# Performance work log

Hardware: AMD Instinct MI355X
Metric: run time of the kernel (lower is better)

The kernel has to match this reference:

```python
import jax, jax.numpy as jnp
import numpy as np

NB_HEAD = 8
SIZE_PER_HEAD = 64
MAX_LEN = 1024
D_IN = 512
BATCH = 8
NEG_BIG = 1e12  # matches the torch module's mask * 1000000000000.0


def setup_inputs() -> dict:
    key = jax.random.key(0)
    ks = jax.random.split(key, 6)
    return {
        "Q_seq": jax.random.normal(ks[0], (BATCH, MAX_LEN, D_IN), dtype=jnp.float32),
        "K_seq": jax.random.normal(ks[1], (BATCH, MAX_LEN, D_IN), dtype=jnp.float32),
        "V_seq": jax.random.normal(ks[2], (BATCH, MAX_LEN, D_IN), dtype=jnp.float32),
        "WQ": jax.random.normal(ks[3], (D_IN, NB_HEAD * SIZE_PER_HEAD), dtype=jnp.float32),
        "WK": jax.random.normal(ks[4], (D_IN, NB_HEAD * SIZE_PER_HEAD), dtype=jnp.float32),
        "WV": jax.random.normal(ks[5], (D_IN, NB_HEAD * SIZE_PER_HEAD), dtype=jnp.float32),
    }


def reference(Q_seq, K_seq, V_seq, WQ, WK, WV):
    B, L, _ = Q_seq.shape
    H, D = NB_HEAD, SIZE_PER_HEAD
    # QKV projections -> [B, H, L, D]
    q = (Q_seq @ WQ).reshape(B, L, H, D).transpose(0, 2, 1, 3)
    k = (K_seq @ WK).reshape(B, L, H, D).transpose(0, 2, 1, 3)
    v = (V_seq @ WV).reshape(B, L, H, D).transpose(0, 2, 1, 3)
    # scaled dot-product scores [B, H, Lq, Lk]
    scores = jnp.einsum("bhqd,bhkd->bhqk", q, k) / jnp.sqrt(jnp.float32(D))
    # causal mask: the torch Mask() subtracts 1e12 where key_idx > query_idx
    causal = jnp.triu(jnp.ones((L, L), dtype=scores.dtype), k=1)  # 1 where k > q
    scores = scores - causal[None, None, :, :] * NEG_BIG
    attn = jax.nn.softmax(scores, axis=-1)
    out = jnp.einsum("bhqk,bhkd->bhqd", attn, v)  # [B, H, L, D]
    return out.transpose(0, 2, 1, 3).reshape(B, L, H * D)
```

## Files before the change

kernel.cpp:

```cpp
#include <hip/hip_runtime.h>
#include <cstddef>

#define LEN    1024
#define DIN    512
#define NHEAD  8
#define HDIM   64
#define BATCH  8

typedef __attribute__((ext_vector_type(8))) short  short8;
typedef __attribute__((ext_vector_type(4))) float  f32x4;

#define MFMA16(a, b, c) __builtin_amdgcn_mfma_f32_16x16x32_bf16((a), (b), (c), 0, 0, 0)
#define PERM_HI 0x07060302u
#define PERM_LO 0x05040100u

__device__ __forceinline__ unsigned short bf_hi(float x) {
    unsigned u = __float_as_uint(x);
    return (unsigned short)((u + 0x7fffu + ((u >> 16) & 1u)) >> 16);
}
__device__ __forceinline__ void bf_split(float x, unsigned short& h, unsigned short& l) {
    unsigned u  = __float_as_uint(x);
    unsigned hu = (u + 0x7fffu + ((u >> 16) & 1u)) >> 16;
    h = (unsigned short)hu;
    l = bf_hi(x - __uint_as_float(hu << 16));
}
__device__ __forceinline__ void unpack4(uint4 u, ushort4& h, ushort4& l) {
    h = make_ushort4((unsigned short)(u.x >> 16), (unsigned short)(u.y >> 16),
                     (unsigned short)(u.z >> 16), (unsigned short)(u.w >> 16));
    l = make_ushort4((unsigned short)(u.x & 0xffff), (unsigned short)(u.y & 0xffff),
                     (unsigned short)(u.z & 0xffff), (unsigned short)(u.w & 0xffff));
}
__device__ __forceinline__ void unpack8(uint4 a, uint4 b, uint4& h, uint4& l) {
    h = make_uint4(__builtin_amdgcn_perm(a.y, a.x, PERM_HI),
                   __builtin_amdgcn_perm(a.w, a.z, PERM_HI),
                   __builtin_amdgcn_perm(b.y, b.x, PERM_HI),
                   __builtin_amdgcn_perm(b.w, b.z, PERM_HI));
    l = make_uint4(__builtin_amdgcn_perm(a.y, a.x, PERM_LO),
                   __builtin_amdgcn_perm(a.w, a.z, PERM_LO),
                   __builtin_amdgcn_perm(b.y, b.x, PERM_LO),
                   __builtin_amdgcn_perm(b.w, b.z, PERM_LO));
}

template<int CTRL>
__device__ __forceinline__ float dpp_mov(float x) {
    return __int_as_float(__builtin_amdgcn_update_dpp(
        0, __float_as_int(x), CTRL, 0xF, 0xF, true));
}
__device__ __forceinline__ float red16_max(float x) {
    x = fmaxf(x, dpp_mov<0xB1>(x));
    x = fmaxf(x, dpp_mov<0x4E>(x));
    x = fmaxf(x, dpp_mov<0x141>(x));
    x = fmaxf(x, dpp_mov<0x140>(x));
    return x;
}
__device__ __forceinline__ float red16_sum(float x) {
    x += dpp_mov<0xB1>(x);
    x += dpp_mov<0x4E>(x);
    x += dpp_mov<0x141>(x);
    x += dpp_mov<0x140>(x);
    return x;
}

__global__ __launch_bounds__(256)
void wprep(const float* __restrict__ WQ, const float* __restrict__ WK,
           const float* __restrict__ WV, unsigned short* __restrict__ wt)
{
    __shared__ float T[64][68];
    const int z = blockIdx.z;
    const float* W = (z == 0) ? WQ : (z == 1) ? WK : WV;
    unsigned short* Wth = wt + (size_t)z * 524288;
    unsigned short* Wtl = Wth + 262144;
    const int k0 = blockIdx.x * 64, n0 = blockIdx.y * 64;
    const int t = threadIdx.x;
    #pragma unroll
    for (int e = 0; e < 4; ++e) {
        int f = e * 256 + t, r = f >> 4, c4 = (f & 15) << 2;
        *(float4*)&T[r][c4] = *(const float4*)&W[(size_t)(k0 + r) * 512 + n0 + c4];
    }
    __syncthreads();
    #pragma unroll
    for (int e = 0; e < 4; ++e) {
        int f = e * 256 + t, nr = f >> 4, kc4 = (f & 15) << 2;
        ushort4 h, l;
        bf_split(T[kc4 + 0][nr], h.x, l.x);
        bf_split(T[kc4 + 1][nr], h.y, l.y);
        bf_split(T[kc4 + 2][nr], h.z, l.z);
        bf_split(T[kc4 + 3][nr], h.w, l.w);
        *(ushort4*)&Wth[(size_t)(n0 + nr) * 512 + k0 + kc4] = h;
        *(ushort4*)&Wtl[(size_t)(n0 + nr) * 512 + k0 + kc4] = l;
    }
}

#define PSTR 40

__global__ __launch_bounds__(256, 3)
void proj_mfma(const float* __restrict__ Qin, const float* __restrict__ Kin,
               const float* __restrict__ Vin, const unsigned short* __restrict__ wt,
               unsigned int* __restrict__ qhl, unsigned int* __restrict__ khl,
               unsigned short* __restrict__ vh)
{
    __shared__ unsigned short Ah[128 * PSTR], Al[128 * PSTR],
                              Bh[128 * PSTR], Bl[128 * PSTR];
    const int z = blockIdx.z;
    const bool full = (z < 2);
    const float* X = (z == 0) ? Qin : (z == 1) ? Kin : Vin;
    const unsigned short* Wth = wt + (size_t)z * 524288;
    const unsigned short* Wtl = Wth + 262144;

    const int t = threadIdx.x, lane = t & 63, w = t >> 6;
    const int wm = w & 1, wn = w >> 1;
    const int m0 = blockIdx.x * 128, n0 = blockIdx.y * 128;
    const int lm = lane & 15, lq = lane >> 4;
    const int ar = t >> 1, ak = (t & 1) * 16;

    const float* Xp = X + (size_t)(m0 + ar) * 512 + ak;
    const unsigned short* Bph = Wth + (size_t)(n0 + ar) * 512 + ak;
    const unsigned short* Bpl = Wtl + (size_t)(n0 + ar) * 512 + ak;

    f32x4 acc[4][4];
    #pragma unroll
    for (int i = 0; i < 4; ++i)
        #pragma unroll
        for (int j = 0; j < 4; ++j) acc[i][j] = 0.f;

    float4 av[4];
    uint4 bh0, bh1, bl0, bl1;
    #pragma unroll
    for (int e = 0; e < 4; ++e) av[e] = *(const float4*)(Xp + e * 4);
    bh0 = *(const uint4*)(Bph);
    bh1 = *(const uint4*)(Bph + 8);
    if (full) { bl0 = *(const uint4*)(Bpl); bl1 = *(const uint4*)(Bpl + 8); }

    for (int k0 = 0; k0 < 512; k0 += 32) {
        __syncthreads();
        {
            const float* ff = (const float*)&av[0];
            uint hw[16];
            #pragma unroll
            for (int i = 0; i < 16; ++i) hw[i] = __float_as_uint(ff[i]) & 0xffff0000u;
            uint4 ahv  = make_uint4(__builtin_amdgcn_perm(hw[1],  hw[0],  PERM_HI),
                                    __builtin_amdgcn_perm(hw[3],  hw[2],  PERM_HI),
                                    __builtin_amdgcn_perm(hw[5],  hw[4],  PERM_HI),
                                    __builtin_amdgcn_perm(hw[7],  hw[6],  PERM_HI));
            uint4 ahv2 = make_uint4(__builtin_amdgcn_perm(hw[9],  hw[8],  PERM_HI),
                                    __builtin_amdgcn_perm(hw[11], hw[10], PERM_HI),
                                    __builtin_amdgcn_perm(hw[13], hw[12], PERM_HI),
                                    __builtin_amdgcn_perm(hw[15], hw[14], PERM_HI));
            *(uint4*)&Ah[ar * PSTR + ak]     = ahv;
            *(uint4*)&Ah[ar * PSTR + ak + 8] = ahv2;
            if (full) {
                uint lo[8];
                #pragma unroll
                for (int i = 0; i < 8; ++i) {
                    float r0 = ff[2*i]   - __uint_as_float(hw[2*i]);
                    float r1 = ff[2*i+1] - __uint_as_float(hw[2*i+1]);
                    lo[i] = ((uint)bf_hi(r1) << 16) | bf_hi(r0);
                }
                *(uint4*)&Al[ar * PSTR + ak]     = make_uint4(lo[0], lo[1], lo[2], lo[3]);
                *(uint4*)&Al[ar * PSTR + ak + 8] = make_uint4(lo[4], lo[5], lo[6], lo[7]);
            }
        }
        *(uint4*)&Bh[ar * PSTR + ak]     = bh0;
        *(uint4*)&Bh[ar * PSTR + ak + 8] = bh1;
        if (full) {
            *(uint4*)&Bl[ar * PSTR + ak]     = bl0;
            *(uint4*)&Bl[ar * PSTR + ak + 8] = bl1;
        }
        __syncthreads();

        if (k0 + 32 < 512) {
            #pragma unroll
            for (int e = 0; e < 4; ++e) av[e] = *(const float4*)(Xp + k0 + 32 + e * 4);
            bh0 = *(const uint4*)(Bph + k0 + 32);
            bh1 = *(const uint4*)(Bph + k0 + 40);
            if (full) {
                bl0 = *(const uint4*)(Bpl + k0 + 32);
                bl1 = *(const uint4*)(Bpl + k0 + 40);
            }
        }

        short8 a_h[4], a_l[4];
        #pragma unroll
        for (int mi = 0; mi < 4; ++mi) {
            int off = (wm * 64 + mi * 16 + lm) * PSTR + lq * 8;
            a_h[mi] = *(const short8*)&Ah[off];
            if (full) a_l[mi] = *(const short8*)&Al[off];
        }
        #pragma unroll
        for (int ni = 0; ni < 4; ++ni) {
            int off = (wn * 64 + ni * 16 + lm) * PSTR + lq * 8;
            short8 b_h = *(const short8*)&Bh[off];
            if (full) {
                short8 b_l = *(const short8*)&Bl[off];
                #pragma unroll
                for (int mi = 0; mi < 4; ++mi) {
                    acc[mi][ni] = MFMA16(a_l[mi], b_h, acc[mi][ni]);
                    acc[mi][ni] = MFMA16(a_h[mi], b_l, acc[mi][ni]);
                    acc[mi][ni] = MFMA16(a_h[mi], b_h, acc[mi][ni]);
                }
            } else {
                #pragma unroll
                for (int mi = 0; mi < 4; ++mi)
                    acc[mi][ni] = MFMA16(a_h[mi], b_h, acc[mi][ni]);
            }
        }
    }

    if (z < 2) {
        unsigned int* o = (z == 0) ? qhl : khl;
        const float sc = (z == 0) ? 0.18033688011112042f : 1.0f;
        #pragma unroll
        for (int mi = 0; mi < 4; ++mi)
            #pragma unroll
            for (int ni = 0; ni < 4; ++ni) {
                int n_abs = n0 + wn * 64 + ni * 16 + lm;
                int hd = n_abs >> 6, d = n_abs & 63;
                #pragma unroll
                for (int r = 0; r < 4; ++r) {
                    int m_abs = m0 + wm * 64 + mi * 16 + lq * 4 + r;
                    int b = m_abs >> 10, li = m_abs & 1023;
                    unsigned short hv, lv;
                    bf_split(acc[mi][ni][r] * sc, hv, lv);
                    o[(((size_t)b * NHEAD + hd) * LEN + li) * HDIM + d] =
                        ((unsigned)hv << 16) | lv;
                }
            }
    } else {
        #pragma unroll
        for (int mi = 0; mi < 4; ++mi) {
            int m_base = m0 + wm * 64 + mi * 16 + lq * 4;
            int b = m_base >> 10, l0 = m_base & 1023;
            #pragma unroll
            for (int ni = 0; ni < 4; ++ni) {
                int n_abs = n0 + wn * 64 + ni * 16 + lm;
                int hd = n_abs >> 6, d = n_abs & 63;
                ushort4 hv = make_ushort4(bf_hi(acc[mi][ni][0]), bf_hi(acc[mi][ni][1]),
                                          bf_hi(acc[mi][ni][2]), bf_hi(acc[mi][ni][3]));
                *(ushort4*)&vh[(((size_t)b * NHEAD + hd) * HDIM + d) * LEN + l0] = hv;
            }
        }
    }
}

__global__ __launch_bounds__(256)
void attn_mfma(const unsigned int* __restrict__ qhl, const unsigned int* __restrict__ khl,
               const unsigned short* __restrict__ vth, float* __restrict__ out)
{
    __shared__ unsigned short sm[18432];
    unsigned short* Kh  = sm;
    unsigned short* Kl  = sm + 4608;
    unsigned short* Pb  = sm;
    unsigned short* Vt  = sm + 9216;
    unsigned short* Qsh = sm;
    unsigned short* Qsl = sm + 9216;

    const int t = threadIdx.x, lane = t & 63, w = t >> 6;
    const int lm = lane & 15, lq = lane >> 4;
    const int bx = blockIdx.x;
    const int idx = bx >> 1, par = bx & 1;
    const int bh = idx & 63;
    const int a  = idx >> 6;
    const int qt = par ? (7 - a) : a;
    const size_t base = (size_t)bh * LEN * HDIM;
    const unsigned int*   qb = qhl + base;
    const unsigned int*   kb = khl + base;
    const unsigned short* vb = vth + base;
    const int Q0  = qt * 128;
    const int Q0w = Q0 + w * 32;

    #pragma unroll
    for (int e = 0; e < 8; ++e) {
        int f = e * 256 + t, r = f >> 4, c4 = (f & 15) << 2;
        uint4 u = *(const uint4*)&qb[(size_t)(Q0 + r) * 64 + c4];
        ushort4 h, l;
        unpack4(u, h, l);
        *(ushort4*)&Qsh[r * 72 + c4] = h;
        *(ushort4*)&Qsl[r * 72 + c4] = l;
    }
    __syncthreads();
    short8 qfh[2][2], qfl[2][2];
    #pragma unroll
    for (int mi = 0; mi < 2; ++mi)
        #pragma unroll
        for (int ks = 0; ks < 2; ++ks) {
            int off = (w * 32 + mi * 16 + lm) * 72 + ks * 32 + lq * 8;
            qfh[mi][ks] = *(const short8*)&Qsh[off];
            qfl[mi][ks] = *(const short8*)&Qsl[off];
        }

    float m_i[2][4], l_i[2][4];
    f32x4 oacc[2][4];
    #pragma unroll
    for (int mi = 0; mi < 2; ++mi)
        #pragma unroll
        for (int r = 0; r < 4; ++r) { m_i[mi][r] = -1e30f; l_i[mi][r] = 0.f; }
    #pragma unroll
    for (int mi = 0; mi < 2; ++mi)
        #pragma unroll
        for (int nd = 0; nd < 4; ++nd) oacc[mi][nd] = 0.f;

    const int kr = t >> 2, kq = t & 3;
    const int vd_ = t >> 3, vs8 = (t & 7) << 3;

    uint4 kreg[4], vreg[2];
    #pragma unroll
    for (int e = 0; e < 4; ++e)
        kreg[e] = *(const uint4*)&kb[(size_t)kr * 64 + kq * 16 + e * 4];
    #pragma unroll
    for (int e = 0; e < 2; ++e)
        vreg[e] = *(const uint4*)&vb[(size_t)(e * 32 + vd_) * LEN + vs8];

    const int jend = 2 * qt + 1;
    for (int jb = 0; jb <= jend; ++jb) {
        __syncthreads();
        {
            uint4 h0, l0, h1, l1;
            unpack8(kreg[0], kreg[1], h0, l0);
            unpack8(kreg[2], kreg[3], h1, l1);
            int ko = kr * 72 + kq * 16;
            *(uint4*)&Kh[ko]     = h0;
            *(uint4*)&Kh[ko + 8] = h1;
            *(uint4*)&Kl[ko]     = l0;
            *(uint4*)&Kl[ko + 8] = l1;
            *(uint4*)&Vt[(vd_)      * 72 + vs8] = vreg[0];
            *(uint4*)&Vt[(vd_ + 32) * 72 + vs8] = vreg[1];
        }
        __syncthreads();

        if (jb < jend) {
            #pragma unroll
            for (int e = 0; e < 4; ++e)
                kreg[e] = *(const uint4*)&kb[(size_t)((jb + 1) * 64 + kr) * 64 + kq * 16 + e * 4];
            #pragma unroll
            for (int e = 0; e < 2; ++e)
                vreg[e] = *(const uint4*)&vb[(size_t)(e * 32 + vd_) * LEN + (jb + 1) * 64 + vs8];
        }

        const bool active = (jb * 64 <= Q0w + 31);
        f32x4 sf[2][4];
        if (active) {
            #pragma unroll
            for (int mi = 0; mi < 2; ++mi)
                #pragma unroll
                for (int ni = 0; ni < 4; ++ni) sf[mi][ni] = 0.f;
            #pragma unroll
            for (int ks = 0; ks < 2; ++ks)
                #pragma unroll
                for (int ni = 0; ni < 4; ++ni) {
                    int off = (ni * 16 + lm) * 72 + ks * 32 + lq * 8;
                    short8 b_h = *(const short8*)&Kh[off];
                    short8 b_l = *(const short8*)&Kl[off];
                    #pragma unroll
                    for (int mi = 0; mi < 2; ++mi) {
                        sf[mi][ni] = MFMA16(qfl[mi][ks], b_h, sf[mi][ni]);
                        sf[mi][ni] = MFMA16(qfh[mi][ks], b_l, sf[mi][ni]);
                        sf[mi][ni] = MFMA16(qfh[mi][ks], b_h, sf[mi][ni]);
                    }
                }
            if (jb * 64 + 63 > Q0w) {
                #pragma unroll
                for (int mi = 0; mi < 2; ++mi)
                    #pragma unroll
                    for (int ni = 0; ni < 4; ++ni) {
                        int key = jb * 64 + ni * 16 + lm;
                        #pragma unroll
                        for (int r = 0; r < 4; ++r) {
                            int qi = Q0w + mi * 16 + lq * 4 + r;
                            if (key > qi) sf[mi][ni][r] = -1e30f;
                        }
                    }
            }
        }
        __syncthreads();

        if (active) {
            #pragma unroll
            for (int mi = 0; mi < 2; ++mi)
                #pragma unroll
                for (int r = 0; r < 4; ++r) {
                    float mv = fmaxf(fmaxf(sf[mi][0][r], sf[mi][1][r]),
                                     fmaxf(sf[mi][2][r], sf[mi][3][r]));
                    mv = red16_max(mv);
                    float mo = m_i[mi][r];
                    float mn = fmaxf(mo, mv);
                    float al = __builtin_amdgcn_exp2f(mo - mn);
                    m_i[mi][r] = mn;
                    float rs = 0.f;
                    int prow = (w * 32 + mi * 16 + lq * 4 + r) * 72 + lm;
                    #pragma unroll
                    for (int ni = 0; ni < 4; ++ni) {
                        float p = __builtin_amdgcn_exp2f(sf[mi][ni][r] - mn);
                        rs += p;
                        Pb[prow + ni * 16] = bf_hi(p);
                    }
                    rs = red16_sum(rs);
                    l_i[mi][r] = l_i[mi][r] * al + rs;
                    #pragma unroll
                    for (int nd = 0; nd < 4; ++nd) oacc[mi][nd][r] *= al;
                }
            short8 pf[2][2];
            #pragma unroll
            for (int mi = 0; mi < 2; ++mi)
                #pragma unroll
                for (int ks = 0; ks < 2; ++ks)
                    pf[mi][ks] = *(const short8*)&Pb[(w * 32 + mi * 16 + lm) * 72 + ks * 32 + lq * 8];
            #pragma unroll
            for (int ks = 0; ks < 2; ++ks)
                #pragma unroll
                for (int nd = 0; nd < 4; ++nd) {
                    short8 vf = *(const short8*)&Vt[(nd * 16 + lm) * 72 + ks * 32 + lq * 8];
                    #pragma unroll
                    for (int mi = 0; mi < 2; ++mi)
                        oacc[mi][nd] = MFMA16(pf[mi][ks], vf, oacc[mi][nd]);
                }
        }
    }

    const int b = bh >> 3, hd = bh & 7;
    #pragma unroll
    for (int mi = 0; mi < 2; ++mi)
        #pragma unroll
        for (int r = 0; r < 4; ++r) {
            int qrow = Q0w + mi * 16 + lq * 4 + r;
            float inv = 1.0f / l_i[mi][r];
            #pragma unroll
            for (int nd = 0; nd < 4; ++nd) {
                int d = nd * 16 + lm;
                out[((size_t)b * LEN + qrow) * (NHEAD * HDIM) + hd * 64 + d] =
                    oacc[mi][nd][r] * inv;
            }
        }
}

extern "C" void kernel_launch(void* const* d_in, const int* in_sizes, int n_in,
                              void* d_out, int out_size, void* d_ws, size_t ws_size,
                              hipStream_t stream)
{
    const float* Qin = (const float*)d_in[0];
    const float* Kin = (const float*)d_in[1];
    const float* Vin = (const float*)d_in[2];
    const float* WQ  = (const float*)d_in[3];
    const float* WK  = (const float*)d_in[4];
    const float* WV  = (const float*)d_in[5];

    const size_t per = (size_t)BATCH * NHEAD * LEN * HDIM;
    unsigned int*   qhl = (unsigned int*)d_ws;
    unsigned int*   khl = qhl + per;
    unsigned short* vh  = (unsigned short*)(khl + per);
    unsigned short* wt  = vh + per;

    wprep    <<<dim3(8, 8, 3),  256, 0, stream>>>(WQ, WK, WV, wt);
    proj_mfma<<<dim3(64, 4, 3), 256, 0, stream>>>(Qin, Kin, Vin, wt, qhl, khl, vh);
    attn_mfma<<<dim3(512),      256, 0, stream>>>(qhl, khl, vh, (float*)d_out);
}
```

Measured before the change: 188.0 us.

## Transpose attention MFMA operands so each lane owns a query row

Swaps the MFMA A/B operands for QK^T and PV so score and output accumulators are laid out with one query row per lane. The row max and sum then need only two cross-lane shuffles instead of a 16-lane DPP reduction per element, and the running m/l state shrinks to one value per row tile. P gets its own XOR-swizzled LDS region, written as packed bf16 pairs, so one __syncthreads per key block can be dropped. The output is stored as float4 vectors, and launch bounds now request 3 blocks per CU. The trade-off is a larger shared-memory footprint and possible register pressure from the occupancy hint.

```diff
diff --git a/kernel.cpp b/kernel.cpp
--- a/kernel.cpp
+++ b/kernel.cpp
@@ -40,25 +40,8 @@
                    __builtin_amdgcn_perm(b.y, b.x, PERM_LO),
                    __builtin_amdgcn_perm(b.w, b.z, PERM_LO));
 }
-
-template<int CTRL>
-__device__ __forceinline__ float dpp_mov(float x) {
-    return __int_as_float(__builtin_amdgcn_update_dpp(
-        0, __float_as_int(x), CTRL, 0xF, 0xF, true));
-}
-__device__ __forceinline__ float red16_max(float x) {
-    x = fmaxf(x, dpp_mov<0xB1>(x));
-    x = fmaxf(x, dpp_mov<0x4E>(x));
-    x = fmaxf(x, dpp_mov<0x141>(x));
-    x = fmaxf(x, dpp_mov<0x140>(x));
-    return x;
-}
-__device__ __forceinline__ float red16_sum(float x) {
-    x += dpp_mov<0xB1>(x);
-    x += dpp_mov<0x4E>(x);
-    x += dpp_mov<0x141>(x);
-    x += dpp_mov<0x140>(x);
-    return x;
+__device__ __forceinline__ short8 as_s8(uint4 u) {
+    union { uint4 u; short8 s; } x; x.u = u; return x.s;
 }
 
 __global__ __launch_bounds__(256)
@@ -242,15 +225,15 @@
     }
 }
 
-__global__ __launch_bounds__(256)
+__global__ __launch_bounds__(256, 3)
 void attn_mfma(const unsigned int* __restrict__ qhl, const unsigned int* __restrict__ khl,
                const unsigned short* __restrict__ vth, float* __restrict__ out)
 {
-    __shared__ unsigned short sm[18432];
-    unsigned short* Kh  = sm;
-    unsigned short* Kl  = sm + 4608;
-    unsigned short* Pb  = sm;
-    unsigned short* Vt  = sm + 9216;
+    __shared__ unsigned short sm[23040];
+    unsigned short* Kh = sm;
+    unsigned short* Kl = sm + 4608;
+    unsigned short* Vt = sm + 9216;
+    unsigned int*   Pb = (unsigned int*)(sm + 13824);
     unsigned short* Qsh = sm;
     unsigned short* Qsl = sm + 9216;
 
@@ -288,16 +271,15 @@
             qfl[mi][ks] = *(const short8*)&Qsl[off];
         }
 
-    float m_i[2][4], l_i[2][4];
+    float m_i[2], l_i[2];
     f32x4 oacc[2][4];
     #pragma unroll
-    for (int mi = 0; mi < 2; ++mi)
-        #pragma unroll
-        for (int r = 0; r < 4; ++r) { m_i[mi][r] = -1e30f; l_i[mi][r] = 0.f; }
-    #pragma unroll
-    for (int mi = 0; mi < 2; ++mi)
+    for (int mi = 0; mi < 2; ++mi) {
+        m_i[mi] = -1e30f;
+        l_i[mi] = 0.f;
         #pragma unroll
         for (int nd = 0; nd < 4; ++nd) oacc[mi][nd] = 0.f;
+    }
 
     const int kr = t >> 2, kq = t & 3;
     const int vd_ = t >> 3, vs8 = (t & 7) << 3;
@@ -337,8 +319,8 @@
         }
 
         const bool active = (jb * 64 <= Q0w + 31);
-        f32x4 sf[2][4];
         if (active) {
+            f32x4 sf[2][4];
             #pragma unroll
             for (int mi = 0; mi < 2; ++mi)
                 #pragma unroll
@@ -348,62 +330,82 @@
                 #pragma unroll
                 for (int ni = 0; ni < 4; ++ni) {
                     int off = (ni * 16 + lm) * 72 + ks * 32 + lq * 8;
-                    short8 b_h = *(const short8*)&Kh[off];
-                    short8 b_l = *(const short8*)&Kl[off];
+                    short8 k_h = *(const short8*)&Kh[off];
+                    short8 k_l = *(const short8*)&Kl[off];
                     #pragma unroll
                     for (int mi = 0; mi < 2; ++mi) {
-                        sf[mi][ni] = MFMA16(qfl[mi][ks], b_h, sf[mi][ni]);
-                        sf[mi][ni] = MFMA16(qfh[mi][ks], b_l, sf[mi][ni]);
-                        sf[mi][ni] = MFMA16(qfh[mi][ks], b_h, sf[mi][ni]);
+                        sf[mi][ni] = MFMA16(k_h, qfl[mi][ks], sf[mi][ni]);
+                        sf[mi][ni] = MFMA16(k_l, qfh[mi][ks], sf[mi][ni]);
+                        sf[mi][ni] = MFMA16(k_h, qfh[mi][ks], sf[mi][ni]);
                     }
                 }
             if (jb * 64 + 63 > Q0w) {
                 #pragma unroll
-                for (int mi = 0; mi < 2; ++mi)
+                for (int mi = 0; mi < 2; ++mi) {
+                    int qi = Q0w + mi * 16 + lm;
                     #pragma unroll
                     for (int ni = 0; ni < 4; ++ni) {
-                        int key = jb * 64 + ni * 16 + lm;
+                        int key0 = jb * 64 + ni * 16 + lq * 4;
                         #pragma unroll
-                        for (int r = 0; r < 4; ++r) {
-                            int qi = Q0w + mi * 16 + lq * 4 + r;
-                            if (key > qi) sf[mi][ni][r] = -1e30f;
-                        }
+                        for (int r = 0; r < 4; ++r)
+                            if (key0 + r > qi) sf[mi][ni][r] = -1e30f;
                     }
-            }
-        }
-        __syncthreads();
-
-        if (active) {
-            #pragma unroll
-            for (int mi = 0; mi < 2; ++mi)
-                #pragma unroll
-                for (int r = 0; r < 4; ++r) {
-                    float mv = fmaxf(fmaxf(sf[mi][0][r], sf[mi][1][r]),
-                                     fmaxf(sf[mi][2][r], sf[mi][3][r]));
-                    mv = red16_max(mv);
-                    float mo = m_i[mi][r];
-                    float mn = fmaxf(mo, mv);
-                    float al = __builtin_amdgcn_exp2f(mo - mn);
-                    m_i[mi][r] = mn;
-                    float rs = 0.f;
-                    int prow = (w * 32 + mi * 16 + lq * 4 + r) * 72 + lm;
-                    #pragma unroll
-                    for (int ni = 0; ni < 4; ++ni) {
-                        float p = __builtin_amdgcn_exp2f(sf[mi][ni][r] - mn);
-                        rs += p;
-                        Pb[prow + ni * 16] = bf_hi(p);
-                    }
-                    rs = red16_sum(rs);
-                    l_i[mi][r] = l_i[mi][r] * al + rs;
-                    #pragma unroll
-                    for (int nd = 0; nd < 4; ++nd) oacc[mi][nd][r] *= al;
-                }
+                }
+            }
+
             short8 pf[2][2];
             #pragma unroll
-            for (int mi = 0; mi < 2; ++mi)
-                #pragma unroll
-                for (int ks = 0; ks < 2; ++ks)
-                    pf[mi][ks] = *(const short8*)&Pb[(w * 32 + mi * 16 + lm) * 72 + ks * 32 + lq * 8];
+            for (int mi = 0; mi < 2; ++mi) {
+                int rowl = w * 32 + mi * 16 + lm;
+                unsigned X = (unsigned)(rowl & 3) << 3;
+                unsigned int* prow = Pb + rowl * 36;
+
+                f32x4 m4 = sf[mi][0];
+                #pragma unroll
+                for (int ni = 1; ni < 4; ++ni) {
+                    m4[0] = fmaxf(m4[0], sf[mi][ni][0]);
+                    m4[1] = fmaxf(m4[1], sf[mi][ni][1]);
+                    m4[2] = fmaxf(m4[2], sf[mi][ni][2]);
+                    m4[3] = fmaxf(m4[3], sf[mi][ni][3]);
+                }
+                float mv = fmaxf(fmaxf(m4[0], m4[1]), fmaxf(m4[2], m4[3]));
+                mv = fmaxf(mv, __shfl_xor(mv, 16));
+                mv = fmaxf(mv, __shfl_xor(mv, 32));
+                float mo = m_i[mi];
+                float mn = fmaxf(mo, mv);
+                float al = __builtin_amdgcn_exp2f(mo - mn);
+                m_i[mi] = mn;
+
+                float rs = 0.f;
+                #pragma unroll
+                for (int ni = 0; ni < 4; ++ni) {
+                    float p0 = __builtin_amdgcn_exp2f(sf[mi][ni][0] - mn);
+                    float p1 = __builtin_amdgcn_exp2f(sf[mi][ni][1] - mn);
+                    float p2 = __builtin_amdgcn_exp2f(sf[mi][ni][2] - mn);
+                    float p3 = __builtin_amdgcn_exp2f(sf[mi][ni][3] - mn);
+                    rs += (p0 + p1) + (p2 + p3);
+                    unsigned col = 8u * ni + 2u * lq;
+                    prow[(col ^ X)]     = ((uint)bf_hi(p1) << 16) | bf_hi(p0);
+                    prow[(col ^ X) + 1] = ((uint)bf_hi(p3) << 16) | bf_hi(p2);
+                }
+                rs += __shfl_xor(rs, 16);
+                rs += __shfl_xor(rs, 32);
+                l_i[mi] = l_i[mi] * al + rs;
+                #pragma unroll
+                for (int nd = 0; nd < 4; ++nd) {
+                    oacc[mi][nd][0] *= al;
+                    oacc[mi][nd][1] *= al;
+                    oacc[mi][nd][2] *= al;
+                    oacc[mi][nd][3] *= al;
+                }
+                #pragma unroll
+                for (int ks = 0; ks < 2; ++ks) {
+                    unsigned cb = ((unsigned)(16 * ks + 4 * lq)) ^ X;
+                    uint4 pu = *(const uint4*)&prow[cb];
+                    pf[mi][ks] = as_s8(pu);
+                }
+            }
+
             #pragma unroll
             for (int ks = 0; ks < 2; ++ks)
                 #pragma unroll
@@ -411,25 +413,24 @@
                     short8 vf = *(const short8*)&Vt[(nd * 16 + lm) * 72 + ks * 32 + lq * 8];
                     #pragma unroll
                     for (int mi = 0; mi < 2; ++mi)
-                        oacc[mi][nd] = MFMA16(pf[mi][ks], vf, oacc[mi][nd]);
+                        oacc[mi][nd] = MFMA16(vf, pf[mi][ks], oacc[mi][nd]);
                 }
         }
     }
 
     const int b = bh >> 3, hd = bh & 7;
     #pragma unroll
-    for (int mi = 0; mi < 2; ++mi)
-        #pragma unroll
-        for (int r = 0; r < 4; ++r) {
-            int qrow = Q0w + mi * 16 + lq * 4 + r;
-            float inv = 1.0f / l_i[mi][r];
-            #pragma unroll
-            for (int nd = 0; nd < 4; ++nd) {
-                int d = nd * 16 + lm;
-                out[((size_t)b * LEN + qrow) * (NHEAD * HDIM) + hd * 64 + d] =
-                    oacc[mi][nd][r] * inv;
-            }
-        }
+    for (int mi = 0; mi < 2; ++mi) {
+        int qrow = Q0w + mi * 16 + lm;
+        float inv = 1.0f / l_i[mi];
+        #pragma unroll
+        for (int nd = 0; nd < 4; ++nd) {
+            float4 o = make_float4(oacc[mi][nd][0] * inv, oacc[mi][nd][1] * inv,
+                                   oacc[mi][nd][2] * inv, oacc[mi][nd][3] * inv);
+            *(float4*)&out[((size_t)b * LEN + qrow) * (NHEAD * HDIM)
+                           + hd * 64 + nd * 16 + lq * 4] = o;
+        }
+    }
 }
 
 extern "C" void kernel_launch(void* const* d_in, const int* in_sizes, int n_in,
```

After: 194.7 us. +3.6%, slower.
